# Kernel tuning notes

Hardware: AMD Instinct MI355X
Metric: run time of the kernel (lower is better)

## Reference

```python
import jax, jax.numpy as jnp
import numpy as np

D_MODEL = 1024
D_STATE = 16
D_CONV = 4
EXPAND = 2
DT_RANK = 64
D_INNER = EXPAND * D_MODEL
B, L = 1, 2048


def setup_inputs() -> dict:
    key = jax.random.key(0)
    ks = jax.random.split(key, 10)
    x = jax.random.normal(ks[0], (B, L, D_MODEL), dtype=jnp.float32)
    # linear weights (stored as [out, in], like torch)
    W_in = jax.random.normal(ks[1], (2 * D_INNER, D_MODEL), dtype=jnp.float32) * (1.0 / np.sqrt(D_MODEL))
    conv_w = jax.random.normal(ks[2], (D_INNER, 1, D_CONV), dtype=jnp.float32) * (1.0 / np.sqrt(D_CONV))
    conv_b = jax.random.normal(ks[3], (D_INNER,), dtype=jnp.float32) * 0.02
    W_x = jax.random.normal(ks[4], (DT_RANK + 2 * D_STATE, D_INNER), dtype=jnp.float32) * (1.0 / np.sqrt(D_INNER))
    W_dt = jax.random.normal(ks[5], (D_INNER, DT_RANK), dtype=jnp.float32) * (1.0 / np.sqrt(DT_RANK))
    # dt bias init: inverse-softplus of dt ~ LogUniform(1e-3, 0.1)
    dt = jnp.exp(jax.random.uniform(ks[6], (D_INNER,)) * (np.log(0.1) - np.log(0.001)) + np.log(0.001))
    dt = jnp.clip(dt, 1e-4, None)
    b_dt = dt + jnp.log(-jnp.expm1(-dt))
    # A_log init: log(1..d_state) broadcast over d_inner
    A_log = jnp.log(jnp.broadcast_to(jnp.arange(1, D_STATE + 1, dtype=jnp.float32)[None, :], (D_INNER, D_STATE)))
    D_param = jnp.ones((D_INNER,), dtype=jnp.float32)
    W_out = jax.random.normal(ks[7], (D_MODEL, D_INNER), dtype=jnp.float32) * (1.0 / np.sqrt(D_INNER))
    return dict(x=x, W_in=W_in, conv_w=conv_w, conv_b=conv_b, W_x=W_x,
                W_dt=W_dt, b_dt=b_dt, A_log=A_log, D_param=D_param, W_out=W_out)


def _silu(v):
    return v * jax.nn.sigmoid(v)


def _mamba_forward(x, W_in, conv_w, conv_b, W_x, W_dt, b_dt, A_log, D_param, W_out):
    # in_proj: (B, L, 2*d_inner)
    xz = jnp.einsum('bld,ed->ble', x, W_in)
    x_in, z = jnp.split(xz, 2, axis=-1)  # each (B, L, d_inner)

    # depthwise causal conv1d (torch pads d_conv-1 both sides then truncates -> causal left pad)
    xc = jnp.transpose(x_in, (0, 2, 1))  # (B, d_inner, L)
    xc = jax.lax.conv_general_dilated(
        xc, conv_w,
        window_strides=(1,), padding=[(D_CONV - 1, 0)],
        dimension_numbers=('NCH', 'OIH', 'NCH'),
        feature_group_count=D_INNER)
    xc = xc + conv_b[None, :, None]
    x_conv = _silu(jnp.transpose(xc, (0, 2, 1)))  # (B, L, d_inner)

    # selective SSM
    A = -jnp.exp(A_log)  # (d_inner, d_state)
    x_dbl = jnp.einsum('bld,ed->ble', x_conv, W_x)  # (B, L, dt_rank + 2*d_state)
    dt_low, B_ssm, C = jnp.split(x_dbl, [DT_RANK, DT_RANK + D_STATE], axis=-1)
    dt = jax.nn.softplus(jnp.einsum('blr,dr->bld', dt_low, W_dt) + b_dt)  # (B, L, d_inner)

    dA = jnp.exp(jnp.einsum('bld,dn->bldn', dt, A))                        # (B, L, d_inner, d_state)
    dBx = dt[..., None] * B_ssm[:, :, None, :] * x_conv[..., None]          # dB * x, (B, L, d_inner, d_state)

    def step(h, inp):
        dA_t, dBx_t, C_t = inp          # (B, d, n), (B, d, n), (B, n)
        h = dA_t * h + dBx_t
        y_t = jnp.einsum('bdn,bn->bd', h, C_t)
        return h, y_t

    h0 = jnp.zeros((x.shape[0], D_INNER, D_STATE), dtype=x.dtype)
    xs = (jnp.swapaxes(dA, 0, 1), jnp.swapaxes(dBx, 0, 1), jnp.swapaxes(C, 0, 1))
    _, ys = jax.lax.scan(step, h0, xs)   # ys: (L, B, d_inner)
    y = jnp.swapaxes(ys, 0, 1) + x_conv * D_param  # (B, L, d_inner)

    y = y * _silu(z)
    return jnp.einsum('bld,ed->ble', y, W_out)  # (B, L, d_model)


def reference(x, W_in, conv_w, conv_b, W_x, W_dt, b_dt, A_log, D_param, W_out):
    return _mamba_forward(x, W_in, conv_w, conv_b, W_x, W_dt, b_dt, A_log, D_param, W_out)
```

## Files before the change

kernel.cpp:

```cpp
#include <hip/hip_runtime.h>
#include <math.h>

#define LSEQ   2048
#define DMODEL 1024
#define DINNER 2048
#define DSTATE 16
#define DTRANK 64
#define XCOLS  96
#define CL     32
#define NC     (LSEQ/CL)
#define SSTATE (DINNER*DSTATE)

typedef __attribute__((ext_vector_type(8))) short bf16x8;
typedef __attribute__((ext_vector_type(4))) float f32x4;
typedef unsigned short ushort_t;
typedef unsigned int uint_t;

__device__ __forceinline__ float siluf(float v) { return v / (1.f + __expf(-v)); }

__device__ __forceinline__ ushort_t f2bf(float f) {
    uint_t u = __float_as_uint(f);
    u += 0x7FFFu + ((u >> 16) & 1u);
    return (ushort_t)(u >> 16);
}

__device__ __forceinline__ bf16x8 cvt8(float4 lo, float4 hi) {
    bf16x8 r;
    r[0] = (short)f2bf(lo.x); r[1] = (short)f2bf(lo.y);
    r[2] = (short)f2bf(lo.z); r[3] = (short)f2bf(lo.w);
    r[4] = (short)f2bf(hi.x); r[5] = (short)f2bf(hi.y);
    r[6] = (short)f2bf(hi.z); r[7] = (short)f2bf(hi.w);
    return r;
}

__global__ __launch_bounds__(256)
void cast5_kernel(const float* __restrict__ s0, ushort_t* __restrict__ d0, int c0,
                  const float* __restrict__ s1, ushort_t* __restrict__ d1, int c1,
                  const float* __restrict__ s2, ushort_t* __restrict__ d2, int c2,
                  const float* __restrict__ s3, ushort_t* __restrict__ d3, int c3,
                  const float* __restrict__ s4, ushort_t* __restrict__ d4, int c4)
{
    int i = (blockIdx.x * 256 + threadIdx.x) * 8;
    const float* s; ushort_t* d;
    if (i < c0)                { s = s0 + i;                  d = d0 + i; }
    else if (i < c0+c1)        { s = s1 + (i-c0);             d = d1 + (i-c0); }
    else if (i < c0+c1+c2)     { s = s2 + (i-c0-c1);          d = d2 + (i-c0-c1); }
    else if (i < c0+c1+c2+c3)  { s = s3 + (i-c0-c1-c2);       d = d3 + (i-c0-c1-c2); }
    else if (i < c0+c1+c2+c3+c4) { s = s4 + (i-c0-c1-c2-c3);  d = d4 + (i-c0-c1-c2-c3); }
    else return;
    *(bf16x8*)d = cvt8(*(const float4*)s, *(const float4*)(s + 4));
}

__device__ __forceinline__ void stage_tile(const ushort_t* __restrict__ A,
                                           const ushort_t* __restrict__ B,
                                           ushort_t* As, ushort_t* Bs,
                                           int m0, int n0, int K, int k0, int tid)
{
#pragma unroll
    for (int j = 0; j < 2; j++) {
        const int c   = j * 256 + tid;
        const int row = c & 127;
        const int kbi = c >> 7;
        __builtin_amdgcn_global_load_lds(
            (const __attribute__((address_space(1))) uint_t*)(A + (size_t)(m0 + row) * K + k0 + kbi * 8),
            (__attribute__((address_space(3))) uint_t*)((char*)As + c * 16), 16, 0, 0);
        __builtin_amdgcn_global_load_lds(
            (const __attribute__((address_space(1))) uint_t*)(B + (size_t)(n0 + row) * K + k0 + kbi * 8),
            (__attribute__((address_space(3))) uint_t*)((char*)Bs + c * 16), 16, 0, 0);
    }
}

__global__ __launch_bounds__(256)
void gemm_bf16(const ushort_t* __restrict__ A,
               const ushort_t* __restrict__ B,
               float* __restrict__ C, int M, int N, int K)
{
    __shared__ ushort_t As[2][4096];
    __shared__ ushort_t Bs[2][4096];

    const int tid  = threadIdx.x;
    const int wid  = tid >> 6;
    const int lane = tid & 63;
    const int m0 = blockIdx.x * 128;
    const int n0 = blockIdx.y * 128;
    const int NT = K / 32;
    const int wr = (wid >> 1) * 64;
    const int wc = (wid & 1) * 64;
    const int lr = lane & 15;
    const int kbq = lane >> 4;

    f32x4 acc[4][4];
#pragma unroll
    for (int m = 0; m < 4; m++)
#pragma unroll
        for (int n = 0; n < 4; n++)
            acc[m][n] = (f32x4){0.f, 0.f, 0.f, 0.f};

    stage_tile(A, B, As[0], Bs[0], m0, n0, K, 0, tid);

    for (int t = 0; t < NT; t++) {
        const int cur = t & 1;
        if (t + 1 < NT) {
            stage_tile(A, B, As[cur ^ 1], Bs[cur ^ 1], m0, n0, K, (t + 1) * 32, tid);
            asm volatile("s_waitcnt vmcnt(4)" ::: "memory");
        } else {
            asm volatile("s_waitcnt vmcnt(0)" ::: "memory");
        }
        __builtin_amdgcn_s_barrier();
        __builtin_amdgcn_sched_barrier(0);

        bf16x8 af[4], bfr[4];
#pragma unroll
        for (int m = 0; m < 4; m++)
            af[m] = *(const bf16x8*)&As[cur][(kbq * 128 + wr + m * 16 + lr) * 8];
#pragma unroll
        for (int n = 0; n < 4; n++)
            bfr[n] = *(const bf16x8*)&Bs[cur][(kbq * 128 + wc + n * 16 + lr) * 8];
#pragma unroll
        for (int m = 0; m < 4; m++)
#pragma unroll
            for (int n = 0; n < 4; n++)
                acc[m][n] = __builtin_amdgcn_mfma_f32_16x16x32_bf16(af[m], bfr[n], acc[m][n], 0, 0, 0);

        __builtin_amdgcn_sched_barrier(0);
        __builtin_amdgcn_s_barrier();
    }

    const int er = (lane >> 4) * 4;
    const int ec = lane & 15;
#pragma unroll
    for (int m = 0; m < 4; m++) {
        const int grow = m0 + wr + m * 16 + er;
#pragma unroll
        for (int n = 0; n < 4; n++) {
            const int gcol = n0 + wc + n * 16 + ec;
#pragma unroll
            for (int r = 0; r < 4; r++)
                C[(size_t)(grow + r) * N + gcol] = acc[m][n][r];
        }
    }
}

__global__ __launch_bounds__(256)
void gemm_xdbl(const ushort_t* __restrict__ A,
               const ushort_t* __restrict__ B,
               float* __restrict__ Cout)
{
    const int tid = threadIdx.x, wid = tid >> 6, lane = tid & 63;
    const int m0 = blockIdx.x * 128;
    const int kbase = blockIdx.z * 128;
    const int wr = (wid >> 1) * 64;
    const int wc = (wid & 1) * 48;
    const int lr = lane & 15;
    const int kq = (lane >> 4) * 8;

    f32x4 acc[4][3];
#pragma unroll
    for (int m = 0; m < 4; m++)
#pragma unroll
        for (int n = 0; n < 3; n++)
            acc[m][n] = (f32x4){0.f, 0.f, 0.f, 0.f};

#pragma unroll
    for (int ks = 0; ks < 4; ks++) {
        const int k0 = kbase + ks * 32;
        bf16x8 af[4], bfr[3];
#pragma unroll
        for (int m = 0; m < 4; m++)
            af[m] = *(const bf16x8*)(A + (size_t)(m0 + wr + m * 16 + lr) * DINNER + k0 + kq);
#pragma unroll
        for (int n = 0; n < 3; n++)
            bfr[n] = *(const bf16x8*)(B + (size_t)(wc + n * 16 + lr) * DINNER + k0 + kq);
#pragma unroll
        for (int m = 0; m < 4; m++)
#pragma unroll
            for (int n = 0; n < 3; n++)
                acc[m][n] = __builtin_amdgcn_mfma_f32_16x16x32_bf16(af[m], bfr[n], acc[m][n], 0, 0, 0);
    }

    const int er = (lane >> 4) * 4;
    const int ec = lane & 15;
#pragma unroll
    for (int m = 0; m < 4; m++)
#pragma unroll
        for (int n = 0; n < 3; n++)
#pragma unroll
            for (int r = 0; r < 4; r++)
                atomicAdd(&Cout[(size_t)(m0 + wr + m * 16 + er + r) * XCOLS + wc + n * 16 + ec],
                          acc[m][n][r]);
}

__global__ __launch_bounds__(256)
void gemm_dt(const float* __restrict__ Axd,
             const ushort_t* __restrict__ Bw,
             const float* __restrict__ bias,
             float* __restrict__ dtm)
{
    const int tid = threadIdx.x, wid = tid >> 6, lane = tid & 63;
    const int m0 = blockIdx.x * 128;
    const int n0 = blockIdx.y * 128;
    const int wr = (wid >> 1) * 64;
    const int wc = (wid & 1) * 64;
    const int lr = lane & 15;
    const int kq = (lane >> 4) * 8;

    f32x4 acc[4][4];
#pragma unroll
    for (int m = 0; m < 4; m++)
#pragma unroll
        for (int n = 0; n < 4; n++)
            acc[m][n] = (f32x4){0.f, 0.f, 0.f, 0.f};

#pragma unroll
    for (int kk = 0; kk < 2; kk++) {
        bf16x8 af[4], bfr[4];
#pragma unroll
        for (int m = 0; m < 4; m++) {
            const float* p = Axd + (size_t)(m0 + wr + m * 16 + lr) * XCOLS + kk * 32 + kq;
            af[m] = cvt8(*(const float4*)p, *(const float4*)(p + 4));
        }
#pragma unroll
        for (int n = 0; n < 4; n++)
            bfr[n] = *(const bf16x8*)(Bw + (size_t)(n0 + wc + n * 16 + lr) * DTRANK + kk * 32 + kq);
#pragma unroll
        for (int m = 0; m < 4; m++)
#pragma unroll
            for (int n = 0; n < 4; n++)
                acc[m][n] = __builtin_amdgcn_mfma_f32_16x16x32_bf16(af[m], bfr[n], acc[m][n], 0, 0, 0);
    }

    const int er = (lane >> 4) * 4;
    const int ec = lane & 15;
#pragma unroll
    for (int m = 0; m < 4; m++)
#pragma unroll
        for (int n = 0; n < 4; n++) {
            const int gcol = n0 + wc + n * 16 + ec;
            const float bv = bias[gcol];
#pragma unroll
            for (int r = 0; r < 4; r++) {
                float c = acc[m][n][r] + bv;
                c = (c > 20.f) ? c : log1pf(__expf(c));
                dtm[(size_t)(m0 + wr + m * 16 + er + r) * DINNER + gcol] = c;
            }
        }
}

__global__ __launch_bounds__(256)
void conv_silu_kernel(const float* __restrict__ xz,
                      const float* __restrict__ conv_w,
                      const float* __restrict__ conv_b,
                      float* __restrict__ xc,
                      ushort_t* __restrict__ xcb)
{
    int idx = blockIdx.x * 256 + threadIdx.x;
    if (idx >= LSEQ * DINNER) return;
    int t = idx / DINNER;
    int d = idx - t * DINNER;
    float acc = conv_b[d];
#pragma unroll
    for (int j = 0; j < 4; j++) {
        int tt = t - 3 + j;
        if (tt >= 0) acc = fmaf(conv_w[d*4 + j], xz[(size_t)tt * (2*DINNER) + d], acc);
    }
    float v = siluf(acc);
    xc[idx] = v;
    xcb[idx] = f2bf(v);
}

__global__ __launch_bounds__(256)
void scan_phase1(const float* __restrict__ dtm,
                 const float* __restrict__ xdbl,
                 const float* __restrict__ xc,
                 const float* __restrict__ A_log,
                 float* __restrict__ Aprod, float* __restrict__ hend)
{
    __shared__ float Bs[CL][16];
    const int tid = threadIdx.x;
    const int d = blockIdx.x * 256 + tid;
    const int c = blockIdx.y;
    const int t0 = c * CL;

    {
        int t = tid >> 3, n = (tid * 2) & 15;
        float2 v = *(const float2*)&xdbl[(size_t)(t0 + t) * XCOLS + DTRANK + n];
        Bs[t][n] = v.x; Bs[t][n + 1] = v.y;
    }

    float a[16];
#pragma unroll
    for (int q = 0; q < 4; q++) {
        f32x4 v = *(const f32x4*)&A_log[(size_t)d * DSTATE + q * 4];
#pragma unroll
        for (int j = 0; j < 4; j++) a[q * 4 + j] = -__expf(v[j]);
    }
    float h[16];
#pragma unroll
    for (int n = 0; n < 16; n++) h[n] = 0.f;
    float sdt = 0.f;

    __syncthreads();

    float dtv = dtm[(size_t)t0 * DINNER + d];
    float xv  = xc[(size_t)t0 * DINNER + d];
    for (int tt = 0; tt < CL; tt++) {
        int tn_ = t0 + ((tt + 1 < CL) ? tt + 1 : tt);
        float dtv_n = dtm[(size_t)tn_ * DINNER + d];
        float xv_n  = xc[(size_t)tn_ * DINNER + d];

        f32x4 Bq[4];
#pragma unroll
        for (int q = 0; q < 4; q++) Bq[q] = *(const f32x4*)&Bs[tt][q * 4];
        float dtx = dtv * xv;
        sdt += dtv;
#pragma unroll
        for (int n = 0; n < 16; n++) {
            float e = __expf(dtv * a[n]);
            h[n] = fmaf(e, h[n], dtx * Bq[n >> 2][n & 3]);
        }
        dtv = dtv_n; xv = xv_n;
    }

#pragma unroll
    for (int n = 0; n < 16; n++) {
        const size_t k = (size_t)c * SSTATE + (size_t)n * DINNER + d;
        hend[k]  = h[n];
        Aprod[k] = __expf(a[n] * sdt);
    }
}

__global__ __launch_bounds__(256)
void scan_phase2(const float* __restrict__ Aprod, float* __restrict__ hend)
{
    const int idx = blockIdx.x * 256 + threadIdx.x;
    float carry = 0.f;
#pragma unroll
    for (int c = 0; c < NC; c++) {
        const size_t k = (size_t)c * SSTATE + idx;
        float oh = hend[k];
        float oA = Aprod[k];
        hend[k] = carry;
        carry = fmaf(oA, carry, oh);
    }
}

__global__ __launch_bounds__(256)
void scan_phase3(const float* __restrict__ dtm,
                 const float* __restrict__ xdbl,
                 const float* __restrict__ xc,
                 const float* __restrict__ A_log,
                 const float* __restrict__ Dp,
                 const float* __restrict__ xz,
                 const float* __restrict__ hinit,
                 ushort_t* __restrict__ yb)
{
    __shared__ float Bs[CL][16];
    __shared__ float Cs[CL][16];
    const int tid = threadIdx.x;
    const int d = blockIdx.x * 256 + tid;
    const int c = blockIdx.y;
    const int t0 = c * CL;

    {
        int r = tid & 127;
        int t = r >> 2, n = (r * 4) & 15;
        const float* src = &xdbl[(size_t)(t0 + t) * XCOLS + DTRANK + ((tid < 128) ? 0 : DSTATE) + n];
        float4 v = *(const float4*)src;
        float* dst = (tid < 128) ? &Bs[t][n] : &Cs[t][n];
        dst[0] = v.x; dst[1] = v.y; dst[2] = v.z; dst[3] = v.w;
    }

    float a[16];
#pragma unroll
    for (int q = 0; q < 4; q++) {
        f32x4 v = *(const f32x4*)&A_log[(size_t)d * DSTATE + q * 4];
#pragma unroll
        for (int j = 0; j < 4; j++) a[q * 4 + j] = -__expf(v[j]);
    }
    const float Dv = Dp[d];
    float h[16];
#pragma unroll
    for (int n = 0; n < 16; n++)
        h[n] = hinit[(size_t)c * SSTATE + (size_t)n * DINNER + d];

    __syncthreads();

    float dtv = dtm[(size_t)t0 * DINNER + d];
    float xv  = xc[(size_t)t0 * DINNER + d];
    for (int tt = 0; tt < CL; tt++) {
        const int t = t0 + tt;
        int tn_ = t0 + ((tt + 1 < CL) ? tt + 1 : tt);
        float dtv_n = dtm[(size_t)tn_ * DINNER + d];
        float xv_n  = xc[(size_t)tn_ * DINNER + d];
        float zv    = xz[(size_t)t * (2 * DINNER) + DINNER + d];

        f32x4 Bq[4], Cq[4];
#pragma unroll
        for (int q = 0; q < 4; q++) {
            Bq[q] = *(const f32x4*)&Bs[tt][q * 4];
            Cq[q] = *(const f32x4*)&Cs[tt][q * 4];
        }
        float dtx = dtv * xv;
        float y = 0.f;
#pragma unroll
        for (int n = 0; n < 16; n++) {
            float e = __expf(dtv * a[n]);
            h[n] = fmaf(e, h[n], dtx * Bq[n >> 2][n & 3]);
            y = fmaf(h[n], Cq[n >> 2][n & 3], y);
        }
        yb[(size_t)t * DINNER + d] = f2bf((y + Dv * xv) * siluf(zv));
        dtv = dtv_n; xv = xv_n;
    }
}

extern "C" void kernel_launch(void* const* d_in, const int* in_sizes, int n_in,
                              void* d_out, int out_size, void* d_ws, size_t ws_size,
                              hipStream_t stream)
{
    const float* x      = (const float*)d_in[0];
    const float* W_in   = (const float*)d_in[1];
    const float* conv_w = (const float*)d_in[2];
    const float* conv_b = (const float*)d_in[3];
    const float* W_x    = (const float*)d_in[4];
    const float* W_dt   = (const float*)d_in[5];
    const float* b_dt   = (const float*)d_in[6];
    const float* A_log  = (const float*)d_in[7];
    const float* D_par  = (const float*)d_in[8];
    const float* W_out  = (const float*)d_in[9];
    float* out = (float*)d_out;
    float* ws  = (float*)d_ws;

    float* xz    = ws;
    float* xc    = xz   + (size_t)LSEQ * 2 * DINNER;
    float* xdbl  = xc   + (size_t)LSEQ * DINNER;
    float* dtm   = xdbl + (size_t)LSEQ * XCOLS;
    float* Aprod = dtm  + (size_t)LSEQ * DINNER;
    float* hend  = Aprod + (size_t)NC * SSTATE;
    ushort_t* xb   = (ushort_t*)(hend + (size_t)NC * SSTATE);
    ushort_t* Wib  = xb  + (size_t)LSEQ * DMODEL;
    ushort_t* Wob  = Wib + (size_t)(2*DINNER) * DMODEL;
    ushort_t* yb   = Wob + (size_t)DMODEL * DINNER;
    ushort_t* Wxb  = yb  + (size_t)LSEQ * DINNER;
    ushort_t* Wdtb = Wxb + (size_t)XCOLS * DINNER;
    ushort_t* xcb  = (ushort_t*)Aprod;

    {
        int c0 = LSEQ * DMODEL, c1 = 2 * DINNER * DMODEL, c2 = DMODEL * DINNER;
        int c3 = XCOLS * DINNER, c4 = DINNER * DTRANK;
        int total = c0 + c1 + c2 + c3 + c4;
        hipLaunchKernelGGL(cast5_kernel, dim3((total / 8 + 255) / 256), dim3(256), 0, stream,
                           x, xb, c0, W_in, Wib, c1, W_out, Wob, c2,
                           W_x, Wxb, c3, W_dt, Wdtb, c4);
    }

    hipLaunchKernelGGL(gemm_bf16, dim3(LSEQ/128, (2*DINNER)/128), dim3(256), 0, stream,
                       xb, Wib, xz, LSEQ, 2*DINNER, DMODEL);

    hipLaunchKernelGGL(conv_silu_kernel, dim3((LSEQ*DINNER)/256), dim3(256), 0, stream,
                       xz, conv_w, conv_b, xc, xcb);

    hipMemsetAsync(xdbl, 0, (size_t)LSEQ * XCOLS * sizeof(float), stream);
    hipLaunchKernelGGL(gemm_xdbl, dim3(LSEQ/128, 1, 16), dim3(256), 0, stream,
                       xcb, Wxb, xdbl);

    hipLaunchKernelGGL(gemm_dt, dim3(LSEQ/128, DINNER/128), dim3(256), 0, stream,
                       xdbl, Wdtb, b_dt, dtm);

    hipLaunchKernelGGL(scan_phase1, dim3(DINNER/256, NC), dim3(256), 0, stream,
                       dtm, xdbl, xc, A_log, Aprod, hend);
    hipLaunchKernelGGL(scan_phase2, dim3(SSTATE/256), dim3(256), 0, stream,
                       Aprod, hend);
    hipLaunchKernelGGL(scan_phase3, dim3(DINNER/256, NC), dim3(256), 0, stream,
                       dtm, xdbl, xc, A_log, D_par, xz, hend, yb);

    hipLaunchKernelGGL(gemm_bf16, dim3(LSEQ/128, DMODEL/128), dim3(256), 0, stream,
                       yb, Wob, out, LSEQ, DMODEL, DINNER);
}
```

Baseline: 221.9 us.

## Split-K the out-projection GEMM eightfold and split the in-projection GEMM in two

Templates the bf16 GEMM on a split-K factor so each block covers a K slice and writes its own partial-output buffer. The out-projection originally had only 128 blocks, so it now runs as 8 K-slices written into workspace and summed by a new add kernel. The in-projection is issued as two half-K launches, and the conv and scan kernels add the two partial results when reading. This raises block count for the small-N GEMM at the cost of writing and re-reading 8 partial outputs, plus one extra GEMM launch and extra reads for the in-projection.

```diff
diff --git a/kernel.cpp b/kernel.cpp
--- a/kernel.cpp
+++ b/kernel.cpp
@@ -70,6 +70,7 @@
     }
 }
 
+template<int SPLITK>
 __global__ __launch_bounds__(256)
 void gemm_bf16(const ushort_t* __restrict__ A,
                const ushort_t* __restrict__ B,
@@ -83,7 +84,10 @@
     const int lane = tid & 63;
     const int m0 = blockIdx.x * 128;
     const int n0 = blockIdx.y * 128;
-    const int NT = K / 32;
+    const int kcnt  = K / SPLITK;
+    const int kbase = (SPLITK > 1) ? blockIdx.z * kcnt : 0;
+    const int NT = kcnt / 32;
+    float* Cp = C + (size_t)blockIdx.z * M * N;
     const int wr = (wid >> 1) * 64;
     const int wc = (wid & 1) * 64;
     const int lr = lane & 15;
@@ -96,12 +100,12 @@
         for (int n = 0; n < 4; n++)
             acc[m][n] = (f32x4){0.f, 0.f, 0.f, 0.f};
 
-    stage_tile(A, B, As[0], Bs[0], m0, n0, K, 0, tid);
+    stage_tile(A, B, As[0], Bs[0], m0, n0, K, kbase, tid);
 
     for (int t = 0; t < NT; t++) {
         const int cur = t & 1;
         if (t + 1 < NT) {
-            stage_tile(A, B, As[cur ^ 1], Bs[cur ^ 1], m0, n0, K, (t + 1) * 32, tid);
+            stage_tile(A, B, As[cur ^ 1], Bs[cur ^ 1], m0, n0, K, kbase + (t + 1) * 32, tid);
             asm volatile("s_waitcnt vmcnt(4)" ::: "memory");
         } else {
             asm volatile("s_waitcnt vmcnt(0)" ::: "memory");
@@ -136,9 +140,23 @@
             const int gcol = n0 + wc + n * 16 + ec;
 #pragma unroll
             for (int r = 0; r < 4; r++)
-                C[(size_t)(grow + r) * N + gcol] = acc[m][n][r];
-        }
-    }
+                Cp[(size_t)(grow + r) * N + gcol] = acc[m][n][r];
+        }
+    }
+}
+
+__global__ __launch_bounds__(256)
+void add8_kernel(const float* __restrict__ parts, float* __restrict__ out, int n)
+{
+    int i = (blockIdx.x * 256 + threadIdx.x) * 4;
+    if (i >= n) return;
+    float4 s = *(const float4*)(parts + i);
+#pragma unroll
+    for (int p = 1; p < 8; p++) {
+        float4 v = *(const float4*)(parts + (size_t)p * n + i);
+        s.x += v.x; s.y += v.y; s.z += v.z; s.w += v.w;
+    }
+    *(float4*)(out + i) = s;
 }
 
 __global__ __launch_bounds__(256)
@@ -248,6 +266,7 @@
 
 __global__ __launch_bounds__(256)
 void conv_silu_kernel(const float* __restrict__ xz,
+                      const float* __restrict__ xz1, int addz,
                       const float* __restrict__ conv_w,
                       const float* __restrict__ conv_b,
                       float* __restrict__ xc,
@@ -261,7 +280,11 @@
 #pragma unroll
     for (int j = 0; j < 4; j++) {
         int tt = t - 3 + j;
-        if (tt >= 0) acc = fmaf(conv_w[d*4 + j], xz[(size_t)tt * (2*DINNER) + d], acc);
+        if (tt >= 0) {
+            float v = xz[(size_t)tt * (2*DINNER) + d];
+            if (addz) v += xz1[(size_t)tt * (2*DINNER) + d];
+            acc = fmaf(conv_w[d*4 + j], v, acc);
+        }
     }
     float v = siluf(acc);
     xc[idx] = v;
@@ -351,6 +374,7 @@
                  const float* __restrict__ A_log,
                  const float* __restrict__ Dp,
                  const float* __restrict__ xz,
+                 const float* __restrict__ xz1, int addz,
                  const float* __restrict__ hinit,
                  ushort_t* __restrict__ yb)
 {
@@ -393,6 +417,7 @@
         float dtv_n = dtm[(size_t)tn_ * DINNER + d];
         float xv_n  = xc[(size_t)tn_ * DINNER + d];
         float zv    = xz[(size_t)t * (2 * DINNER) + DINNER + d];
+        if (addz) zv += xz1[(size_t)t * (2 * DINNER) + DINNER + d];
 
         f32x4 Bq[4], Cq[4];
 #pragma unroll
@@ -443,6 +468,10 @@
     ushort_t* Wxb  = yb  + (size_t)LSEQ * DINNER;
     ushort_t* Wdtb = Wxb + (size_t)XCOLS * DINNER;
     ushort_t* xcb  = (ushort_t*)Aprod;
+    float* xz1 = (float*)(Wdtb + (size_t)DINNER * DTRANK);
+    const size_t need = (size_t)((char*)(xz1 + (size_t)LSEQ * 2 * DINNER) - (char*)ws);
+    const int use_sk2 = (ws_size >= need) ? 1 : 0;
+    float* outp = ws;
 
     {
         int c0 = LSEQ * DMODEL, c1 = 2 * DINNER * DMODEL, c2 = DMODEL * DINNER;
@@ -453,11 +482,18 @@
                            W_x, Wxb, c3, W_dt, Wdtb, c4);
     }
 
-    hipLaunchKernelGGL(gemm_bf16, dim3(LSEQ/128, (2*DINNER)/128), dim3(256), 0, stream,
-                       xb, Wib, xz, LSEQ, 2*DINNER, DMODEL);
+    if (use_sk2) {
+        hipLaunchKernelGGL((gemm_bf16<2>), dim3(LSEQ/128, (2*DINNER)/128, 1), dim3(256), 0, stream,
+                           xb, Wib, xz, LSEQ, 2*DINNER, DMODEL);
+        hipLaunchKernelGGL((gemm_bf16<2>), dim3(LSEQ/128, (2*DINNER)/128, 1), dim3(256), 0, stream,
+                           xb + DMODEL/2, Wib + DMODEL/2, xz1, LSEQ, 2*DINNER, DMODEL);
+    } else {
+        hipLaunchKernelGGL((gemm_bf16<1>), dim3(LSEQ/128, (2*DINNER)/128, 1), dim3(256), 0, stream,
+                           xb, Wib, xz, LSEQ, 2*DINNER, DMODEL);
+    }
 
     hipLaunchKernelGGL(conv_silu_kernel, dim3((LSEQ*DINNER)/256), dim3(256), 0, stream,
-                       xz, conv_w, conv_b, xc, xcb);
+                       xz, xz1, use_sk2, conv_w, conv_b, xc, xcb);
 
     hipMemsetAsync(xdbl, 0, (size_t)LSEQ * XCOLS * sizeof(float), stream);
     hipLaunchKernelGGL(gemm_xdbl, dim3(LSEQ/128, 1, 16), dim3(256), 0, stream,
@@ -471,8 +507,10 @@
     hipLaunchKernelGGL(scan_phase2, dim3(SSTATE/256), dim3(256), 0, stream,
                        Aprod, hend);
     hipLaunchKernelGGL(scan_phase3, dim3(DINNER/256, NC), dim3(256), 0, stream,
-                       dtm, xdbl, xc, A_log, D_par, xz, hend, yb);
-
-    hipLaunchKernelGGL(gemm_bf16, dim3(LSEQ/128, DMODEL/128), dim3(256), 0, stream,
-                       yb, Wob, out, LSEQ, DMODEL, DINNER);
-}
+                       dtm, xdbl, xc, A_log, D_par, xz, xz1, use_sk2, hend, yb);
+
+    hipLaunchKernelGGL((gemm_bf16<8>), dim3(LSEQ/128, DMODEL/128, 8), dim3(256), 0, stream,
+                       yb, Wob, outp, LSEQ, DMODEL, DINNER);
+    hipLaunchKernelGGL(add8_kernel, dim3((LSEQ*DMODEL/4)/256), dim3(256), 0, stream,
+                       outp, out, LSEQ*DMODEL);
+}
```

Result: no change. 219.7 us (-1.0%).

## Store intermediates in bf16, fuse silu(z) into in_proj epilogue, remap blocks across XCDs

Applied to the files above, without the earlier changes.

The in_proj GEMM epilogue now writes the x half as bf16 and the z half as bf16 silu(z), so the fp32 xz buffer disappears. Conv output, dt and the gate are kept only in bf16 and read as bf16 by the scan kernels. The xdbl memset is folded into the cast kernel, and the GEMM blocks get an XCD-aware swizzle intended to improve L2 reuse. Together these cut intermediate memory traffic and one launch, at the cost of bf16 rounding of dt and x_conv inside the recurrence.

```diff
diff --git a/kernel.cpp b/kernel.cpp
--- a/kernel.cpp
+++ b/kernel.cpp
@@ -23,6 +23,9 @@
     u += 0x7FFFu + ((u >> 16) & 1u);
     return (ushort_t)(u >> 16);
 }
+__device__ __forceinline__ float bf2f(ushort_t u) {
+    return __uint_as_float((uint_t)u << 16);
+}
 
 __device__ __forceinline__ bf16x8 cvt8(float4 lo, float4 hi) {
     bf16x8 r;
@@ -33,22 +36,39 @@
     return r;
 }
 
-__global__ __launch_bounds__(256)
-void cast5_kernel(const float* __restrict__ s0, ushort_t* __restrict__ d0, int c0,
+__device__ __forceinline__ void xcd_remap(int& bx, int& by)
+{
+    const int gx = gridDim.x, gy = gridDim.y;
+    const int flat = blockIdx.x + gx * blockIdx.y;
+    const int q = (gx * gy) >> 3;
+    const int swz = (flat & 7) * q + (flat >> 3);
+    bx = swz % gx;
+    by = swz / gx;
+}
+
+__global__ __launch_bounds__(256)
+void cast6_kernel(const float* __restrict__ s0, ushort_t* __restrict__ d0, int c0,
                   const float* __restrict__ s1, ushort_t* __restrict__ d1, int c1,
                   const float* __restrict__ s2, ushort_t* __restrict__ d2, int c2,
                   const float* __restrict__ s3, ushort_t* __restrict__ d3, int c3,
-                  const float* __restrict__ s4, ushort_t* __restrict__ d4, int c4)
+                  const float* __restrict__ s4, ushort_t* __restrict__ d4, int c4,
+                  float* __restrict__ z0, int cz)
 {
     int i = (blockIdx.x * 256 + threadIdx.x) * 8;
-    const float* s; ushort_t* d;
-    if (i < c0)                { s = s0 + i;                  d = d0 + i; }
-    else if (i < c0+c1)        { s = s1 + (i-c0);             d = d1 + (i-c0); }
-    else if (i < c0+c1+c2)     { s = s2 + (i-c0-c1);          d = d2 + (i-c0-c1); }
-    else if (i < c0+c1+c2+c3)  { s = s3 + (i-c0-c1-c2);       d = d3 + (i-c0-c1-c2); }
-    else if (i < c0+c1+c2+c3+c4) { s = s4 + (i-c0-c1-c2-c3);  d = d4 + (i-c0-c1-c2-c3); }
-    else return;
-    *(bf16x8*)d = cvt8(*(const float4*)s, *(const float4*)(s + 4));
+    int tot = c0 + c1 + c2 + c3 + c4;
+    if (i < tot) {
+        const float* s; ushort_t* d;
+        if (i < c0)                { s = s0 + i;                  d = d0 + i; }
+        else if (i < c0+c1)        { s = s1 + (i-c0);             d = d1 + (i-c0); }
+        else if (i < c0+c1+c2)     { s = s2 + (i-c0-c1);          d = d2 + (i-c0-c1); }
+        else if (i < c0+c1+c2+c3)  { s = s3 + (i-c0-c1-c2);       d = d3 + (i-c0-c1-c2); }
+        else                       { s = s4 + (i-c0-c1-c2-c3);    d = d4 + (i-c0-c1-c2-c3); }
+        *(bf16x8*)d = cvt8(*(const float4*)s, *(const float4*)(s + 4));
+    } else if (i < tot + cz) {
+        float* z = z0 + (i - tot);
+        *(float4*)z       = make_float4(0.f, 0.f, 0.f, 0.f);
+        *(float4*)(z + 4) = make_float4(0.f, 0.f, 0.f, 0.f);
+    }
 }
 
 __device__ __forceinline__ void stage_tile(const ushort_t* __restrict__ A,
@@ -70,19 +90,26 @@
     }
 }
 
+template<int EPI>
 __global__ __launch_bounds__(256)
 void gemm_bf16(const ushort_t* __restrict__ A,
                const ushort_t* __restrict__ B,
-               float* __restrict__ C, int M, int N, int K)
+               float* __restrict__ C,
+               ushort_t* __restrict__ Xb,
+               ushort_t* __restrict__ Gz,
+               int M, int N, int K)
 {
     __shared__ ushort_t As[2][4096];
     __shared__ ushort_t Bs[2][4096];
+
+    int bx, by;
+    xcd_remap(bx, by);
 
     const int tid  = threadIdx.x;
     const int wid  = tid >> 6;
     const int lane = tid & 63;
-    const int m0 = blockIdx.x * 128;
-    const int n0 = blockIdx.y * 128;
+    const int m0 = bx * 128;
+    const int n0 = by * 128;
     const int NT = K / 32;
     const int wr = (wid >> 1) * 64;
     const int wc = (wid & 1) * 64;
@@ -128,15 +155,35 @@
 
     const int er = (lane >> 4) * 4;
     const int ec = lane & 15;
-#pragma unroll
-    for (int m = 0; m < 4; m++) {
-        const int grow = m0 + wr + m * 16 + er;
-#pragma unroll
-        for (int n = 0; n < 4; n++) {
-            const int gcol = n0 + wc + n * 16 + ec;
-#pragma unroll
-            for (int r = 0; r < 4; r++)
-                C[(size_t)(grow + r) * N + gcol] = acc[m][n][r];
+    if (EPI == 0) {
+#pragma unroll
+        for (int m = 0; m < 4; m++) {
+            const int grow = m0 + wr + m * 16 + er;
+#pragma unroll
+            for (int n = 0; n < 4; n++) {
+                const int gcol = n0 + wc + n * 16 + ec;
+#pragma unroll
+                for (int r = 0; r < 4; r++)
+                    C[(size_t)(grow + r) * N + gcol] = acc[m][n][r];
+            }
+        }
+    } else {
+        const bool xside = (n0 < DINNER);
+#pragma unroll
+        for (int m = 0; m < 4; m++) {
+            const int grow = m0 + wr + m * 16 + er;
+#pragma unroll
+            for (int n = 0; n < 4; n++) {
+                const int gcol = n0 + wc + n * 16 + ec;
+#pragma unroll
+                for (int r = 0; r < 4; r++) {
+                    float v = acc[m][n][r];
+                    if (xside)
+                        Xb[(size_t)(grow + r) * DINNER + gcol] = f2bf(v);
+                    else
+                        Gz[(size_t)(grow + r) * DINNER + (gcol - DINNER)] = f2bf(siluf(v));
+                }
+            }
         }
     }
 }
@@ -194,7 +241,7 @@
 void gemm_dt(const float* __restrict__ Axd,
              const ushort_t* __restrict__ Bw,
              const float* __restrict__ bias,
-             float* __restrict__ dtm)
+             ushort_t* __restrict__ dtmb)
 {
     const int tid = threadIdx.x, wid = tid >> 6, lane = tid & 63;
     const int m0 = blockIdx.x * 128;
@@ -241,16 +288,15 @@
             for (int r = 0; r < 4; r++) {
                 float c = acc[m][n][r] + bv;
                 c = (c > 20.f) ? c : log1pf(__expf(c));
-                dtm[(size_t)(m0 + wr + m * 16 + er + r) * DINNER + gcol] = c;
+                dtmb[(size_t)(m0 + wr + m * 16 + er + r) * DINNER + gcol] = f2bf(c);
             }
         }
 }
 
 __global__ __launch_bounds__(256)
-void conv_silu_kernel(const float* __restrict__ xz,
+void conv_silu_kernel(const ushort_t* __restrict__ xinb,
                       const float* __restrict__ conv_w,
                       const float* __restrict__ conv_b,
-                      float* __restrict__ xc,
                       ushort_t* __restrict__ xcb)
 {
     int idx = blockIdx.x * 256 + threadIdx.x;
@@ -261,17 +307,16 @@
 #pragma unroll
     for (int j = 0; j < 4; j++) {
         int tt = t - 3 + j;
-        if (tt >= 0) acc = fmaf(conv_w[d*4 + j], xz[(size_t)tt * (2*DINNER) + d], acc);
-    }
-    float v = siluf(acc);
-    xc[idx] = v;
-    xcb[idx] = f2bf(v);
-}
-
-__global__ __launch_bounds__(256)
-void scan_phase1(const float* __restrict__ dtm,
+        if (tt >= 0)
+            acc = fmaf(conv_w[d*4 + j], bf2f(xinb[(size_t)tt * DINNER + d]), acc);
+    }
+    xcb[idx] = f2bf(siluf(acc));
+}
+
+__global__ __launch_bounds__(256)
+void scan_phase1(const ushort_t* __restrict__ dtmb,
                  const float* __restrict__ xdbl,
-                 const float* __restrict__ xc,
+                 const ushort_t* __restrict__ xcb,
                  const float* __restrict__ A_log,
                  float* __restrict__ Aprod, float* __restrict__ hend)
 {
@@ -301,12 +346,12 @@
 
     __syncthreads();
 
-    float dtv = dtm[(size_t)t0 * DINNER + d];
-    float xv  = xc[(size_t)t0 * DINNER + d];
+    float dtv = bf2f(dtmb[(size_t)t0 * DINNER + d]);
+    float xv  = bf2f(xcb[(size_t)t0 * DINNER + d]);
     for (int tt = 0; tt < CL; tt++) {
         int tn_ = t0 + ((tt + 1 < CL) ? tt + 1 : tt);
-        float dtv_n = dtm[(size_t)tn_ * DINNER + d];
-        float xv_n  = xc[(size_t)tn_ * DINNER + d];
+        float dtv_n = bf2f(dtmb[(size_t)tn_ * DINNER + d]);
+        float xv_n  = bf2f(xcb[(size_t)tn_ * DINNER + d]);
 
         f32x4 Bq[4];
 #pragma unroll
@@ -345,12 +390,12 @@
 }
 
 __global__ __launch_bounds__(256)
-void scan_phase3(const float* __restrict__ dtm,
+void scan_phase3(const ushort_t* __restrict__ dtmb,
                  const float* __restrict__ xdbl,
-                 const float* __restrict__ xc,
+                 const ushort_t* __restrict__ xcb,
                  const float* __restrict__ A_log,
                  const float* __restrict__ Dp,
-                 const float* __restrict__ xz,
+                 const ushort_t* __restrict__ gz,
                  const float* __restrict__ hinit,
                  ushort_t* __restrict__ yb)
 {
@@ -385,14 +430,14 @@
 
     __syncthreads();
 
-    float dtv = dtm[(size_t)t0 * DINNER + d];
-    float xv  = xc[(size_t)t0 * DINNER + d];
+    float dtv = bf2f(dtmb[(size_t)t0 * DINNER + d]);
+    float xv  = bf2f(xcb[(size_t)t0 * DINNER + d]);
     for (int tt = 0; tt < CL; tt++) {
         const int t = t0 + tt;
         int tn_ = t0 + ((tt + 1 < CL) ? tt + 1 : tt);
-        float dtv_n = dtm[(size_t)tn_ * DINNER + d];
-        float xv_n  = xc[(size_t)tn_ * DINNER + d];
-        float zv    = xz[(size_t)t * (2 * DINNER) + DINNER + d];
+        float dtv_n = bf2f(dtmb[(size_t)tn_ * DINNER + d]);
+        float xv_n  = bf2f(xcb[(size_t)tn_ * DINNER + d]);
+        float gzv   = bf2f(gz[(size_t)t * DINNER + d]);
 
         f32x4 Bq[4], Cq[4];
 #pragma unroll
@@ -408,7 +453,7 @@
             h[n] = fmaf(e, h[n], dtx * Bq[n >> 2][n & 3]);
             y = fmaf(h[n], Cq[n >> 2][n & 3], y);
         }
-        yb[(size_t)t * DINNER + d] = f2bf((y + Dv * xv) * siluf(zv));
+        yb[(size_t)t * DINNER + d] = f2bf((y + Dv * xv) * gzv);
         dtv = dtv_n; xv = xv_n;
     }
 }
@@ -430,49 +475,50 @@
     float* out = (float*)d_out;
     float* ws  = (float*)d_ws;
 
-    float* xz    = ws;
-    float* xc    = xz   + (size_t)LSEQ * 2 * DINNER;
-    float* xdbl  = xc   + (size_t)LSEQ * DINNER;
-    float* dtm   = xdbl + (size_t)LSEQ * XCOLS;
-    float* Aprod = dtm  + (size_t)LSEQ * DINNER;
+    float* xdbl  = ws;
+    float* Aprod = xdbl + (size_t)LSEQ * XCOLS;
     float* hend  = Aprod + (size_t)NC * SSTATE;
     ushort_t* xb   = (ushort_t*)(hend + (size_t)NC * SSTATE);
-    ushort_t* Wib  = xb  + (size_t)LSEQ * DMODEL;
-    ushort_t* Wob  = Wib + (size_t)(2*DINNER) * DMODEL;
-    ushort_t* yb   = Wob + (size_t)DMODEL * DINNER;
-    ushort_t* Wxb  = yb  + (size_t)LSEQ * DINNER;
-    ushort_t* Wdtb = Wxb + (size_t)XCOLS * DINNER;
-    ushort_t* xcb  = (ushort_t*)Aprod;
+    ushort_t* Wib  = xb   + (size_t)LSEQ * DMODEL;
+    ushort_t* Wob  = Wib  + (size_t)(2*DINNER) * DMODEL;
+    ushort_t* Wxb  = Wob  + (size_t)DMODEL * DINNER;
+    ushort_t* Wdtb = Wxb  + (size_t)XCOLS * DINNER;
+    ushort_t* xinb = Wdtb + (size_t)DINNER * DTRANK;
+    ushort_t* gz   = xinb + (size_t)LSEQ * DINNER;
+    ushort_t* xcb  = gz   + (size_t)LSEQ * DINNER;
+    ushort_t* dtmb = xcb  + (size_t)LSEQ * DINNER;
+    ushort_t* yb   = dtmb + (size_t)LSEQ * DINNER;
 
     {
         int c0 = LSEQ * DMODEL, c1 = 2 * DINNER * DMODEL, c2 = DMODEL * DINNER;
         int c3 = XCOLS * DINNER, c4 = DINNER * DTRANK;
-        int total = c0 + c1 + c2 + c3 + c4;
-        hipLaunchKernelGGL(cast5_kernel, dim3((total / 8 + 255) / 256), dim3(256), 0, stream,
+        int cz = LSEQ * XCOLS;
+        int total = c0 + c1 + c2 + c3 + c4 + cz;
+        hipLaunchKernelGGL(cast6_kernel, dim3((total / 8 + 255) / 256), dim3(256), 0, stream,
                            x, xb, c0, W_in, Wib, c1, W_out, Wob, c2,
-                           W_x, Wxb, c3, W_dt, Wdtb, c4);
-    }
-
-    hipLaunchKernelGGL(gemm_bf16, dim3(LSEQ/128, (2*DINNER)/128), dim3(256), 0, stream,
-                       xb, Wib, xz, LSEQ, 2*DINNER, DMODEL);
+                           W_x, Wxb, c3, W_dt, Wdtb, c4, xdbl, cz);
+    }
+
+    hipLaunchKernelGGL((gemm_bf16<1>), dim3(LSEQ/128, (2*DINNER)/128), dim3(256), 0, stream,
+                       xb, Wib, (float*)nullptr, xinb, gz, LSEQ, 2*DINNER, DMODEL);
 
     hipLaunchKernelGGL(conv_silu_kernel, dim3((LSEQ*DINNER)/256), dim3(256), 0, stream,
-                       xz, conv_w, conv_b, xc, xcb);
-
-    hipMemsetAsync(xdbl, 0, (size_t)LSEQ * XCOLS * sizeof(float), stream);
+                       xinb, conv_w, conv_b, xcb);
+
     hipLaunchKernelGGL(gemm_xdbl, dim3(LSEQ/128, 1, 16), dim3(256), 0, stream,
                        xcb, Wxb, xdbl);
 
     hipLaunchKernelGGL(gemm_dt, dim3(LSEQ/128, DINNER/128), dim3(256), 0, stream,
-                       xdbl, Wdtb, b_dt, dtm);
+                       xdbl, Wdtb, b_dt, dtmb);
 
     hipLaunchKernelGGL(scan_phase1, dim3(DINNER/256, NC), dim3(256), 0, stream,
-                       dtm, xdbl, xc, A_log, Aprod, hend);
+                       dtmb, xdbl, xcb, A_log, Aprod, hend);
     hipLaunchKernelGGL(scan_phase2, dim3(SSTATE/256), dim3(256), 0, stream,
                        Aprod, hend);
     hipLaunchKernelGGL(scan_phase3, dim3(DINNER/256, NC), dim3(256), 0, stream,
-                       dtm, xdbl, xc, A_log, D_par, xz, hend, yb);
-
-    hipLaunchKernelGGL(gemm_bf16, dim3(LSEQ/128, DMODEL/128), dim3(256), 0, stream,
-                       yb, Wob, out, LSEQ, DMODEL, DINNER);
-}
+                       dtmb, xdbl, xcb, A_log, D_par, gz, hend, yb);
+
+    hipLaunchKernelGGL((gemm_bf16<0>), dim3(LSEQ/128, DMODEL/128), dim3(256), 0, stream,
+                       yb, Wob, out, (ushort_t*)nullptr, (ushort_t*)nullptr,
+                       LSEQ, DMODEL, DINNER);
+}
```

Measured after the change: 220.1 us. About the same (-0.8%).
